# Kernel optimization log

Hardware: AMD Instinct MI355X
Metric: run time of the kernel (lower is better)

Reference implementation:

```python
import jax, jax.numpy as jnp
import numpy as np

B, C, H, W = 4, 192, 128, 128
NH = 6
HD = C // NH            # 32
GS = 8                  # window (group) size
K = 16                  # unfold kernel size
STRIDE, PAD = 8, 4
NUM = H // GS           # 16 groups per side
BG = B * NUM * NUM      # 1024 windows
N = GS * GS             # 64 tokens per group
KK = K * K              # 256 sampled tokens per window
SCALE = HD ** -0.5


def _rope(x):
    # lucidrains-style rotary embedding along dim -2 (positions), last dim = head_dim
    d = x.shape[-1]
    inv = 1.0 / (10000.0 ** (jnp.arange(0, d, 2, dtype=jnp.float32) / d))
    t = jnp.arange(x.shape[-2], dtype=jnp.float32)
    freqs = jnp.repeat(t[:, None] * inv[None, :], 2, axis=-1)  # [seq, d], interleaved
    cos, sin = jnp.cos(freqs), jnp.sin(freqs)
    xp = x.reshape(x.shape[:-1] + (d // 2, 2))
    xr = jnp.stack((-xp[..., 1], xp[..., 0]), axis=-1).reshape(x.shape)
    return x * cos + xr * sin


def _l2norm(x):
    # torch F.normalize(dim=-1): x / max(||x||, eps)
    n = jnp.linalg.norm(x, axis=-1, keepdims=True)
    return x / jnp.maximum(n, 1e-12)


def setup_inputs() -> dict:
    key = jax.random.key(0)
    ks = jax.random.split(key, 6)
    return {
        "x_complete": jax.random.normal(ks[0], (B, C, H, W), jnp.float32),
        "graph": jax.random.randint(ks[1], (BG, 1, N, KK), 0, 2) > 0,
        "w_group": jax.random.normal(ks[2], (C, C), jnp.float32) * 0.02,
        "b_group": jnp.zeros((C,), jnp.float32),
        "w_sample": jax.random.normal(ks[3], (2 * C, C), jnp.float32) * 0.02,
        "b_sample": jnp.zeros((2 * C,), jnp.float32),
        "w_proj": jax.random.normal(ks[4], (C, C), jnp.float32) * 0.02,
        "b_proj": jnp.zeros((C,), jnp.float32),
    }


def reference(x_complete, graph, w_group, b_group, w_sample, b_sample, w_proj, b_proj):
    # --- local grouping: [B,C,(numh sh),(numw sw)] -> [(B numh numw), sh*sw, C]
    xg = x_complete.reshape(B, C, NUM, GS, NUM, GS).transpose(0, 2, 4, 3, 5, 1).reshape(BG, N, C)
    # --- proj_group: 1x1 Conv1d over channels, then split heads 'b (h c) n -> b h n c'
    x1 = jnp.einsum('bnc,dc->bnd', xg, w_group) + b_group
    x1 = x1.reshape(BG, N, NH, HD).transpose(0, 2, 1, 3)            # [BG,NH,N,HD]
    # --- proj_sample: 1x1 Conv2d to 2C channels
    xs = jnp.einsum('bchw,dc->bdhw', x_complete, w_sample) + b_sample[None, :, None, None]
    # --- F.unfold(kernel=16, stride=8, pad=4): patch features channel-major (c,k0,k1)
    patches = jax.lax.conv_general_dilated_patches(
        xs, (K, K), (STRIDE, STRIDE), ((PAD, PAD), (PAD, PAD)))    # [B, 2C*KK, NUM, NUM]
    xs = patches.reshape(B, 2 * C, KK, NUM * NUM).transpose(0, 3, 2, 1).reshape(BG, KK, 2 * C)
    # --- 'b n (div h c) -> div b h n c'
    xs = xs.reshape(BG, KK, 2, NH, HD)
    x2 = xs[:, :, 0].transpose(0, 2, 1, 3)                          # [BG,NH,KK,HD]
    feat = xs[:, :, 1].transpose(0, 2, 1, 3)                        # [BG,NH,KK,HD]
    # --- RoPE + masked cosine-sim attention
    q = _rope(x1)
    k = _rope(x2)
    sim = jnp.einsum('bhmc,bhnc->bhmn', _l2norm(q), _l2norm(k))
    sim = sim + (-100.0) * (~graph).astype(sim.dtype)
    corr = jax.nn.softmax(sim * SCALE, axis=-1)                     # [BG,NH,N,KK]
    out = jnp.einsum('bhmn,bhnc->bhmc', corr, feat)                 # [BG,NH,N,HD]
    out = out.transpose(0, 2, 1, 3).reshape(BG, N, C)
    return out @ w_proj.T + b_proj
```

## Files before the change

### kernel.cpp

```cpp
#include <hip/hip_runtime.h>
#include <hip/hip_bf16.h>

#define B_    4
#define C_    192
#define C2_   384
#define PIX_  16384
#define NH_   6
#define BG_   1024
#define SCALE_ 0.17677669529663687f
#define C1_ 0.2550348943f

typedef __attribute__((ext_vector_type(8))) short short8v;
typedef __attribute__((ext_vector_type(4))) float f32x4;

__global__ __launch_bounds__(256, 1)
void k_rope_init(float2* __restrict__ tbl) {
    int e = blockIdx.x * 256 + threadIdx.x;
    if (e >= 4096) return;
    int pos = e >> 4, j = e & 15;
    float freq = powf(10.0f, -0.25f * (float)j);
    float ang = (float)pos * freq;
    float sn, cs;
    sincosf(ang, &sn, &cs);
    tbl[e] = make_float2(cs, sn);
}

__global__ __launch_bounds__(256, 4)
void k_gmask(const int* __restrict__ g, unsigned int* __restrict__ gbits) {
    int e = blockIdx.x * 256 + threadIdx.x;
    const uint4* p = (const uint4*)(g + (size_t)e * 32);
    unsigned int m = 0u;
#pragma unroll
    for (int i = 0; i < 8; ++i) {
        uint4 v = p[i];
        m |= (v.x ? 1u : 0u) << (i * 4);
        m |= (v.y ? 1u : 0u) << (i * 4 + 1);
        m |= (v.z ? 1u : 0u) << (i * 4 + 2);
        m |= (v.w ? 1u : 0u) << (i * 4 + 3);
    }
    gbits[e] = m;
}

__global__ __launch_bounds__(256, 4)
void k_wcast(const float* __restrict__ wsm, const float* __restrict__ wgb,
             const float* __restrict__ wpj, __hip_bfloat16* __restrict__ wb)
{
    int e = (blockIdx.x * 256 + threadIdx.x) * 4;
    float4 v = (e < 73728) ? *(const float4*)(wsm + e)
             : (e < 110592) ? *(const float4*)(wgb + (e - 73728))
                            : *(const float4*)(wpj + (e - 110592));
    union { uint2 u; __hip_bfloat16 h[4]; } pk;
    pk.h[0] = __float2bfloat16(v.x); pk.h[1] = __float2bfloat16(v.y);
    pk.h[2] = __float2bfloat16(v.z); pk.h[3] = __float2bfloat16(v.w);
    *(uint2*)(wb + e) = pk.u;
}

__global__ __launch_bounds__(256, 4)
void k_convm(const float* __restrict__ x, const __hip_bfloat16* __restrict__ wb,
             const float* __restrict__ bsm, const float* __restrict__ bgb,
             const float2* __restrict__ tbl,
             __hip_bfloat16* __restrict__ xsk, __hip_bfloat16* __restrict__ xsv,
             __hip_bfloat16* __restrict__ qbf)
{
    __shared__ __align__(16) char smem[25600];
    const int bid = blockIdx.x;
    const int b = bid >> 8, pt = bid & 255;
    const int px0 = pt * 64;
    const int t = threadIdx.x;

    {
        const int px = t & 63, cq = t >> 6;
        const float* src = x + ((size_t)b * C_ + cq * 48) * PIX_ + px0 + px;
        char* row = smem + px * 400 + cq * 96;
#pragma unroll
        for (int i = 0; i < 6; ++i) {
            union { uint4 u; __hip_bfloat16 h[8]; } pk;
#pragma unroll
            for (int j = 0; j < 8; ++j)
                pk.h[j] = __float2bfloat16(src[(size_t)(i * 8 + j) * PIX_]);
            *(uint4*)(row + i * 16) = pk.u;
        }
    }
    __syncthreads();

    const int w = t >> 6, lane = t & 63;
    const int l15 = lane & 15, g = lane >> 4;
    const int mb = (w & 1) * 32;
    const int nb = (w >> 1) * 32;

    short8v xf0[6], xf1[6];
#pragma unroll
    for (int ks = 0; ks < 6; ++ks) {
        xf0[ks] = *(const short8v*)(smem + (mb + l15) * 400      + ks * 64 + g * 16);
        xf1[ks] = *(const short8v*)(smem + (mb + 16 + l15) * 400 + ks * 64 + g * 16);
    }

    const f32x4 zz = {0.0f, 0.0f, 0.0f, 0.0f};

#pragma unroll
    for (int o2 = 0; o2 < 3; ++o2) {
        const int oct = 3 + o2;
        f32x4 acc00 = zz, acc01 = zz, acc10 = zz, acc11 = zz;
        const __hip_bfloat16* w0 = wb + (size_t)(oct * 64 + nb + l15) * C_;
        const __hip_bfloat16* w1 = w0 + 16 * C_;
#pragma unroll
        for (int ks = 0; ks < 6; ++ks) {
            const short8v b0 = *(const short8v*)(w0 + ks * 32 + g * 8);
            const short8v b1 = *(const short8v*)(w1 + ks * 32 + g * 8);
            acc00 = __builtin_amdgcn_mfma_f32_16x16x32_bf16(xf0[ks], b0, acc00, 0, 0, 0);
            acc01 = __builtin_amdgcn_mfma_f32_16x16x32_bf16(xf0[ks], b1, acc01, 0, 0, 0);
            acc10 = __builtin_amdgcn_mfma_f32_16x16x32_bf16(xf1[ks], b0, acc10, 0, 0, 0);
            acc11 = __builtin_amdgcn_mfma_f32_16x16x32_bf16(xf1[ks], b1, acc11, 0, 0, 0);
        }
        const float bo0 = bsm[oct * 64 + nb + l15];
        const float bo1 = bsm[oct * 64 + nb + 16 + l15];
        union { uint2 u; __hip_bfloat16 h[4]; } p00, p10, p01, p11;
#pragma unroll
        for (int j = 0; j < 4; ++j) {
            p00.h[j] = __float2bfloat16(acc00[j] + bo0);
            p10.h[j] = __float2bfloat16(acc10[j] + bo0);
            p01.h[j] = __float2bfloat16(acc01[j] + bo1);
            p11.h[j] = __float2bfloat16(acc11[j] + bo1);
        }
        __hip_bfloat16* d0 = xsv + (size_t)(b * C_ + o2 * 64 + nb + l15) * PIX_
                                 + px0 + mb + g * 4;
        *(uint2*)d0        = p00.u;
        *(uint2*)(d0 + 16) = p10.u;
        __hip_bfloat16* d1 = d0 + (size_t)16 * PIX_;
        *(uint2*)d1        = p01.u;
        *(uint2*)(d1 + 16) = p11.u;
    }

#pragma unroll
    for (int o2 = 0; o2 < 3; ++o2) {
        const int oct = o2;
        f32x4 a00 = zz, a01 = zz, a10 = zz, a11 = zz;
        const __hip_bfloat16* w0 = wb + (size_t)(oct * 64 + nb + l15) * C_;
        const __hip_bfloat16* w1 = w0 + 16 * C_;
#pragma unroll
        for (int ks = 0; ks < 6; ++ks) {
            const short8v wf0 = *(const short8v*)(w0 + ks * 32 + g * 8);
            const short8v wf1 = *(const short8v*)(w1 + ks * 32 + g * 8);
            a00 = __builtin_amdgcn_mfma_f32_16x16x32_bf16(wf0, xf0[ks], a00, 0, 0, 0);
            a01 = __builtin_amdgcn_mfma_f32_16x16x32_bf16(wf0, xf1[ks], a01, 0, 0, 0);
            a10 = __builtin_amdgcn_mfma_f32_16x16x32_bf16(wf1, xf0[ks], a10, 0, 0, 0);
            a11 = __builtin_amdgcn_mfma_f32_16x16x32_bf16(wf1, xf1[ks], a11, 0, 0, 0);
        }
        const float4 bv0 = *(const float4*)(bsm + oct * 64 + nb + g * 4);
        const float4 bv1 = *(const float4*)(bsm + oct * 64 + nb + 16 + g * 4);
        a00[0] += bv0.x; a00[1] += bv0.y; a00[2] += bv0.z; a00[3] += bv0.w;
        a01[0] += bv0.x; a01[1] += bv0.y; a01[2] += bv0.z; a01[3] += bv0.w;
        a10[0] += bv1.x; a10[1] += bv1.y; a10[2] += bv1.z; a10[3] += bv1.w;
        a11[0] += bv1.x; a11[1] += bv1.y; a11[2] += bv1.z; a11[3] += bv1.w;
        float s0 = 0.0f, s1 = 0.0f;
#pragma unroll
        for (int j = 0; j < 4; ++j) {
            s0 = fmaf(a00[j], a00[j], s0); s0 = fmaf(a10[j], a10[j], s0);
            s1 = fmaf(a01[j], a01[j], s1); s1 = fmaf(a11[j], a11[j], s1);
        }
        s0 += __shfl_xor(s0, 16); s0 += __shfl_xor(s0, 32);
        s1 += __shfl_xor(s1, 16); s1 += __shfl_xor(s1, 32);
        const float inv0 = 1.0f / fmaxf(sqrtf(s0), 1e-12f);
        const float inv1 = 1.0f / fmaxf(sqrtf(s1), 1e-12f);
        union { uint2 u; __hip_bfloat16 h[4]; } q00, q10, q01, q11;
#pragma unroll
        for (int j = 0; j < 4; ++j) {
            q00.h[j] = __float2bfloat16(a00[j] * inv0);
            q10.h[j] = __float2bfloat16(a10[j] * inv0);
            q01.h[j] = __float2bfloat16(a01[j] * inv1);
            q11.h[j] = __float2bfloat16(a11[j] * inv1);
        }
        __hip_bfloat16* d0 = xsk + ((size_t)b * PIX_ + px0 + mb + l15) * C_
                                 + oct * 64 + nb + g * 4;
        *(uint2*)d0        = q00.u;
        *(uint2*)(d0 + 16) = q10.u;
        __hip_bfloat16* d1 = d0 + (size_t)16 * C_;
        *(uint2*)d1        = q01.u;
        *(uint2*)(d1 + 16) = q11.u;
    }

    const int r = pt >> 1;
    const int c0q = (pt & 1) * 64 + mb + l15;
    const int n0 = (r & 7) * 8 + (c0q & 7);
    const int n1 = (r & 7) * 8 + ((c0q + 16) & 7);
    const int bg0 = (b << 8) + ((r >> 3) << 4) + (c0q >> 3);
    const int bg1 = (b << 8) + ((r >> 3) << 4) + ((c0q + 16) >> 3);
#pragma unroll
    for (int o2 = 0; o2 < 3; ++o2) {
        const int oct = 6 + o2;
        f32x4 a00 = zz, a01 = zz, a10 = zz, a11 = zz;
        const __hip_bfloat16* w0 = wb + (size_t)(oct * 64 + nb + l15) * C_;
        const __hip_bfloat16* w1 = w0 + 16 * C_;
#pragma unroll
        for (int ks = 0; ks < 6; ++ks) {
            const short8v wf0 = *(const short8v*)(w0 + ks * 32 + g * 8);
            const short8v wf1 = *(const short8v*)(w1 + ks * 32 + g * 8);
            a00 = __builtin_amdgcn_mfma_f32_16x16x32_bf16(wf0, xf0[ks], a00, 0, 0, 0);
            a01 = __builtin_amdgcn_mfma_f32_16x16x32_bf16(wf0, xf1[ks], a01, 0, 0, 0);
            a10 = __builtin_amdgcn_mfma_f32_16x16x32_bf16(wf1, xf0[ks], a10, 0, 0, 0);
            a11 = __builtin_amdgcn_mfma_f32_16x16x32_bf16(wf1, xf1[ks], a11, 0, 0, 0);
        }
        const float4 bv0 = *(const float4*)(bgb + (oct - 6) * 64 + nb + g * 4);
        const float4 bv1 = *(const float4*)(bgb + (oct - 6) * 64 + nb + 16 + g * 4);
        a00[0] += bv0.x; a00[1] += bv0.y; a00[2] += bv0.z; a00[3] += bv0.w;
        a01[0] += bv0.x; a01[1] += bv0.y; a01[2] += bv0.z; a01[3] += bv0.w;
        a10[0] += bv1.x; a10[1] += bv1.y; a10[2] += bv1.z; a10[3] += bv1.w;
        a11[0] += bv1.x; a11[1] += bv1.y; a11[2] += bv1.z; a11[3] += bv1.w;
        {
            float2 cA, cB;
            cA = tbl[n0 * 16 + g * 2]; cB = tbl[n0 * 16 + g * 2 + 1];
            { float u0 = a00[0], u1 = a00[1];
              a00[0] = u0 * cA.x - u1 * cA.y; a00[1] = u1 * cA.x + u0 * cA.y; }
            { float u0 = a00[2], u1 = a00[3];
              a00[2] = u0 * cB.x - u1 * cB.y; a00[3] = u1 * cB.x + u0 * cB.y; }
            cA = tbl[n0 * 16 + 8 + g * 2]; cB = tbl[n0 * 16 + 8 + g * 2 + 1];
            { float u0 = a10[0], u1 = a10[1];
              a10[0] = u0 * cA.x - u1 * cA.y; a10[1] = u1 * cA.x + u0 * cA.y; }
            { float u0 = a10[2], u1 = a10[3];
              a10[2] = u0 * cB.x - u1 * cB.y; a10[3] = u1 * cB.x + u0 * cB.y; }
            cA = tbl[n1 * 16 + g * 2]; cB = tbl[n1 * 16 + g * 2 + 1];
            { float u0 = a01[0], u1 = a01[1];
              a01[0] = u0 * cA.x - u1 * cA.y; a01[1] = u1 * cA.x + u0 * cA.y; }
            { float u0 = a01[2], u1 = a01[3];
              a01[2] = u0 * cB.x - u1 * cB.y; a01[3] = u1 * cB.x + u0 * cB.y; }
            cA = tbl[n1 * 16 + 8 + g * 2]; cB = tbl[n1 * 16 + 8 + g * 2 + 1];
            { float u0 = a11[0], u1 = a11[1];
              a11[0] = u0 * cA.x - u1 * cA.y; a11[1] = u1 * cA.x + u0 * cA.y; }
            { float u0 = a11[2], u1 = a11[3];
              a11[2] = u0 * cB.x - u1 * cB.y; a11[3] = u1 * cB.x + u0 * cB.y; }
        }
        float s0 = 0.0f, s1 = 0.0f;
#pragma unroll
        for (int j = 0; j < 4; ++j) {
            s0 = fmaf(a00[j], a00[j], s0); s0 = fmaf(a10[j], a10[j], s0);
            s1 = fmaf(a01[j], a01[j], s1); s1 = fmaf(a11[j], a11[j], s1);
        }
        s0 += __shfl_xor(s0, 16); s0 += __shfl_xor(s0, 32);
        s1 += __shfl_xor(s1, 16); s1 += __shfl_xor(s1, 32);
        const float inv0 = 1.0f / fmaxf(sqrtf(s0), 1e-12f);
        const float inv1 = 1.0f / fmaxf(sqrtf(s1), 1e-12f);
        union { uint2 u; __hip_bfloat16 h[4]; } q00, q10, q01, q11;
#pragma unroll
        for (int j = 0; j < 4; ++j) {
            q00.h[j] = __float2bfloat16(a00[j] * inv0);
            q10.h[j] = __float2bfloat16(a10[j] * inv0);
            q01.h[j] = __float2bfloat16(a01[j] * inv1);
            q11.h[j] = __float2bfloat16(a11[j] * inv1);
        }
        const int hglob = (oct - 6) * 2 + (nb >> 5);
        __hip_bfloat16* d0 = qbf + (((size_t)bg0 * NH_ + hglob) * 64 + n0) * 32 + g * 4;
        *(uint2*)d0        = q00.u;
        *(uint2*)(d0 + 16) = q10.u;
        __hip_bfloat16* d1 = qbf + (((size_t)bg1 * NH_ + hglob) * 64 + n1) * 32 + g * 4;
        *(uint2*)d1        = q01.u;
        *(uint2*)(d1 + 16) = q11.u;
    }
}

__global__ __launch_bounds__(512, 2)
void k_attn(const __hip_bfloat16* __restrict__ xsk, const __hip_bfloat16* __restrict__ xsv,
            const unsigned int* __restrict__ gbits, const __hip_bfloat16* __restrict__ qb,
            const float2* __restrict__ tbl, float* __restrict__ attn)
{
    __shared__ __align__(16) char smem[52736];
    const int bid0 = blockIdx.x;
    const int bid = (bid0 & 7) * 768 + (bid0 >> 3);
    const int h = bid % NH_;
    const int bg = bid / NH_;
    const int b = bg >> 8, ph = (bg >> 4) & 15, pw = bg & 15;
    const int t = threadIdx.x;
    const int w = t >> 6, lane = t & 63;
    const int g = lane >> 4, l15 = lane & 15;
    const int rbase = (w & 3) * 16;
    const int wcol  = w >> 2;
    const int cb    = wcol * 128;
    const int cb32  = wcol * 4;

    const short8v qa = *(const short8v*)(qb +
        ((size_t)(bg * NH_ + h) * 64 + rbase + l15) * 32 + g * 8);

    {
        const int m = t >> 1, half = t & 1;
        const int k0 = m >> 4, k1 = m & 15;
        const int rr = ph * 8 - 4 + k0, cc = pw * 8 - 4 + k1;
        const bool inb = ((unsigned)rr < 128u) && ((unsigned)cc < 128u);
        float kv[16];
        if (inb) {
            const uint4* pk = (const uint4*)(xsk +
                ((size_t)b * PIX_ + rr * 128 + cc) * C_ + h * 32 + half * 16);
            union { uint4 u; __hip_bfloat16 h8[8]; } r0, r1;
            r0.u = pk[0]; r1.u = pk[1];
#pragma unroll
            for (int d = 0; d < 8; ++d) {
                kv[d]     = __bfloat162float(r0.h8[d]);
                kv[8 + d] = __bfloat162float(r1.h8[d]);
            }
        } else {
#pragma unroll
            for (int d = 0; d < 16; ++d) kv[d] = 0.0f;
        }
        union { uint4 u; __hip_bfloat16 hh[8]; } p0, p1;
#pragma unroll
        for (int p = 0; p < 8; ++p) {
            float2 cs = tbl[m * 16 + half * 8 + p];
            float a0 = kv[2 * p], a1 = kv[2 * p + 1];
            float e0 = a0 * cs.x - a1 * cs.y;
            float e1 = a1 * cs.x + a0 * cs.y;
            if (p < 4) { p0.hh[2 * p] = __float2bfloat16(e0); p0.hh[2 * p + 1] = __float2bfloat16(e1); }
            else { p1.hh[2 * (p - 4)] = __float2bfloat16(e0); p1.hh[2 * (p - 4) + 1] = __float2bfloat16(e1); }
        }
        *(uint4*)(smem + m * 80 + half * 32)      = p0.u;
        *(uint4*)(smem + m * 80 + half * 32 + 16) = p1.u;
    }

    {
        const int d = t & 31, k0 = t >> 5;
        const int rr = ph * 8 - 4 + k0;
        const int c0 = pw * 8 - 4;
        char* dst = smem + 34816 + d * 528 + k0 * 32;
        const __hip_bfloat16* src = xsv + (size_t)(b * C_ + h * 32 + d) * PIX_ + rr * 128 + c0;
        const bool rok = (unsigned)rr < 128u;
        if (rok && pw >= 1 && pw <= 14) {
            const uint2* s2 = (const uint2*)src;
            uint2 a0 = s2[0], a1 = s2[1], a2 = s2[2], a3 = s2[3];
            ((uint4*)dst)[0] = make_uint4(a0.x, a0.y, a1.x, a1.y);
            ((uint4*)dst)[1] = make_uint4(a2.x, a2.y, a3.x, a3.y);
        } else {
            __hip_bfloat16* dh = (__hip_bfloat16*)dst;
            __hip_bfloat16 z = __float2bfloat16(0.0f);
#pragma unroll
            for (int i = 0; i < 16; ++i) {
                bool ok = rok && ((unsigned)(c0 + i) < 128u);
                dh[i] = ok ? src[i] : z;
            }
        }
    }

    {
        unsigned int* gbl = (unsigned int*)(smem + 20480);
        const int q = t >> 3, wd = t & 7;
        gbl[q * 9 + wd] = gbits[(size_t)bg * 512 + t];
    }
    __syncthreads();

    f32x4 acc[8];
    const f32x4 zz = {0.0f, 0.0f, 0.0f, 0.0f};
#pragma unroll
    for (int tile = 0; tile < 8; ++tile) {
        const short8v kb = *(const short8v*)(smem + (cb + tile * 16 + l15) * 80 + g * 16);
        acc[tile] = __builtin_amdgcn_mfma_f32_16x16x32_bf16(qa, kb, zz, 0, 0, 0);
    }

    const unsigned int* gbl = (const unsigned int*)(smem + 20480);
    float* reds = (float*)(smem + 51712);
    float sm4[4], inv4[4];
#pragma unroll
    for (int j = 0; j < 4; ++j) {
        const int q = rbase + g * 4 + j;
        const unsigned int wv[4] = { gbl[q * 9 + cb32], gbl[q * 9 + cb32 + 1],
                                     gbl[q * 9 + cb32 + 2], gbl[q * 9 + cb32 + 3] };
        float sm = 0.0f;
#pragma unroll
        for (int tile = 0; tile < 8; ++tile) {
            const unsigned int bit = (wv[tile >> 1] >> ((tile & 1) * 16 + l15)) & 1u;
            float e = __builtin_amdgcn_exp2f(fmaf(acc[tile][j], C1_, -C1_));
            e = bit ? e : 0.0f;
            acc[tile][j] = e;
            sm += e;
        }
        sm += __shfl_xor(sm, 1);
        sm += __shfl_xor(sm, 2);
        sm += __shfl_xor(sm, 4);
        sm += __shfl_xor(sm, 8);
        sm4[j] = sm;
        if (l15 == 0) reds[wcol * 64 + q] = sm;
    }
    __syncthreads();
#pragma unroll
    for (int j = 0; j < 4; ++j) {
        const int q = rbase + g * 4 + j;
        inv4[j] = 1.0f / (sm4[j] + reds[(wcol ^ 1) * 64 + q] + 1e-37f);
    }

    char* plw = smem + w * 4352;
#pragma unroll
    for (int tile = 0; tile < 8; ++tile)
#pragma unroll
        for (int j = 0; j < 4; ++j) {
            *(__hip_bfloat16*)(plw + (g * 4 + j) * 272 + (tile * 16 + l15) * 2) =
                __float2bfloat16(acc[tile][j]);
        }

    f32x4 o0 = zz, o1 = zz;
#pragma unroll
    for (int ks = 0; ks < 4; ++ks) {
        const short8v pa  = *(const short8v*)(plw + l15 * 272 + (ks * 32 + g * 8) * 2);
        const short8v vb0 = *(const short8v*)(smem + 34816 + l15 * 528        + (cb + ks * 32 + g * 8) * 2);
        const short8v vb1 = *(const short8v*)(smem + 34816 + (16 + l15) * 528 + (cb + ks * 32 + g * 8) * 2);
        o0 = __builtin_amdgcn_mfma_f32_16x16x32_bf16(pa, vb0, o0, 0, 0, 0);
        o1 = __builtin_amdgcn_mfma_f32_16x16x32_bf16(pa, vb1, o1, 0, 0, 0);
    }
    __syncthreads();

    float* ob = (float*)smem;
    if (wcol == 1) {
#pragma unroll
        for (int j = 0; j < 4; ++j) {
            const int q = rbase + g * 4 + j;
            ob[q * 33 + l15]      = o0[j];
            ob[q * 33 + 16 + l15] = o1[j];
        }
    }
    __syncthreads();
    if (wcol == 0) {
#pragma unroll
        for (int j = 0; j < 4; ++j) {
            const int q = rbase + g * 4 + j;
            float v0 = (o0[j] + ob[q * 33 + l15])      * inv4[j];
            float v1 = (o1[j] + ob[q * 33 + 16 + l15]) * inv4[j];
            attn[((size_t)bg * 64 + q) * 192 + h * 32 + l15]      = v0;
            attn[((size_t)bg * 64 + q) * 192 + h * 32 + 16 + l15] = v1;
        }
    }
}

__global__ __launch_bounds__(256, 4)
void k_oprojm(const float* __restrict__ attn, const __hip_bfloat16* __restrict__ wpb,
              const float* __restrict__ bp, float* __restrict__ out)
{
    __shared__ __align__(16) char smem[25600];
    const int bid0 = blockIdx.x;
    const int bid = (bid0 & 7) * 384 + (bid0 >> 3);
    const int oct = bid % 3;
    const int rt  = bid / 3;
    const int row0 = rt * 64;
    const int t = threadIdx.x;

#pragma unroll
    for (int e0 = 0; e0 < 12; ++e0) {
        const int e = e0 * 256 + t;
        const int r = e / 48, c4 = e % 48;
        float4 v = *(const float4*)(attn + (size_t)(row0 + r) * 192 + c4 * 4);
        union { uint2 u; __hip_bfloat16 h[4]; } pk;
        pk.h[0] = __float2bfloat16(v.x); pk.h[1] = __float2bfloat16(v.y);
        pk.h[2] = __float2bfloat16(v.z); pk.h[3] = __float2bfloat16(v.w);
        *(uint2*)(smem + r * 400 + c4 * 8) = pk.u;
    }
    __syncthreads();

    const int w = t >> 6, lane = t & 63;
    const int l15 = lane & 15, g = lane >> 4;
    const int mb = (w & 1) * 32;
    const int nb = (w >> 1) * 32;

    const f32x4 zz = {0.0f, 0.0f, 0.0f, 0.0f};
    f32x4 acc00 = zz, acc01 = zz, acc10 = zz, acc11 = zz;
    const __hip_bfloat16* w0 = wpb + (size_t)(oct * 64 + nb + l15) * C_;
    const __hip_bfloat16* w1 = w0 + 16 * C_;
#pragma unroll
    for (int ks = 0; ks < 6; ++ks) {
        const short8v a0 = *(const short8v*)(smem + (mb + l15) * 400      + ks * 64 + g * 16);
        const short8v a1 = *(const short8v*)(smem + (mb + 16 + l15) * 400 + ks * 64 + g * 16);
        const short8v b0 = *(const short8v*)(w0 + ks * 32 + g * 8);
        const short8v b1 = *(const short8v*)(w1 + ks * 32 + g * 8);
        acc00 = __builtin_amdgcn_mfma_f32_16x16x32_bf16(a0, b0, acc00, 0, 0, 0);
        acc01 = __builtin_amdgcn_mfma_f32_16x16x32_bf16(a0, b1, acc01, 0, 0, 0);
        acc10 = __builtin_amdgcn_mfma_f32_16x16x32_bf16(a1, b0, acc10, 0, 0, 0);
        acc11 = __builtin_amdgcn_mfma_f32_16x16x32_bf16(a1, b1, acc11, 0, 0, 0);
    }
    __syncthreads();

    float* ot = (float*)smem;
#pragma unroll
    for (int j = 0; j < 4; ++j) {
        ot[(mb + g * 4 + j) * 68      + nb + l15]      = acc00[j];
        ot[(mb + 16 + g * 4 + j) * 68 + nb + l15]      = acc10[j];
        ot[(mb + g * 4 + j) * 68      + nb + 16 + l15] = acc01[j];
        ot[(mb + 16 + g * 4 + j) * 68 + nb + 16 + l15] = acc11[j];
    }
    __syncthreads();

    {
        const int k = t & 15, pxi = t >> 4;
        const float4 bias4 = *(const float4*)(bp + oct * 64 + k * 4);
#pragma unroll
        for (int p = 0; p < 4; ++p) {
            const int px = p * 16 + pxi;
            float4 v = *(const float4*)&ot[px * 68 + k * 4];
            v.x += bias4.x; v.y += bias4.y; v.z += bias4.z; v.w += bias4.w;
            *(float4*)(out + (size_t)(row0 + px) * 192 + oct * 64 + k * 4) = v;
        }
    }
}

extern "C" void kernel_launch(void* const* d_in, const int* in_sizes, int n_in,
                              void* d_out, int out_size, void* d_ws, size_t ws_size,
                              hipStream_t stream)
{
    (void)in_sizes; (void)n_in; (void)out_size; (void)ws_size;
    const float* x   = (const float*)d_in[0];
    const int* grph  = (const int*)d_in[1];
    const float* wg  = (const float*)d_in[2];
    const float* bgb = (const float*)d_in[3];
    const float* wsm = (const float*)d_in[4];
    const float* bsm = (const float*)d_in[5];
    const float* wp  = (const float*)d_in[6];
    const float* bp  = (const float*)d_in[7];
    float* out = (float*)d_out;

    char* wsb = (char*)d_ws;
    __hip_bfloat16* xsk = (__hip_bfloat16*)wsb;
    __hip_bfloat16* xsv = (__hip_bfloat16*)(wsb + 25165824ull);
    __hip_bfloat16* qbf = (__hip_bfloat16*)(wsb + 50331648ull);
    float2* tbl = (float2*)(wsb + 75497472ull);
    unsigned int* gbits = (unsigned int*)(wsb + 75530240ull);
    __hip_bfloat16* wb  = (__hip_bfloat16*)(wsb + 77627392ull);
    __hip_bfloat16* wpb = wb + 110592;

    hipLaunchKernelGGL(k_rope_init, dim3(16),   dim3(256), 0, stream, tbl);
    hipLaunchKernelGGL(k_wcast,     dim3(144),  dim3(256), 0, stream, wsm, wg, wp, wb);
    hipLaunchKernelGGL(k_gmask,     dim3(2048), dim3(256), 0, stream, grph, gbits);
    hipLaunchKernelGGL(k_convm,     dim3(1024), dim3(256), 0, stream, x, wb, bsm, bgb, tbl, xsk, xsv, qbf);
    hipLaunchKernelGGL(k_attn,      dim3(6144), dim3(512), 0, stream, xsk, xsv, gbits, qbf, tbl, out);
    hipLaunchKernelGGL(k_oprojm,    dim3(3072), dim3(256), 0, stream, out, wpb, bp, out);
}
```

Baseline: 187.4 us.

## Use packed bf16 conversion and transpose score MFMA for row-contiguous softmax

Replaces scalar __float2bfloat16 conversions across all kernels with the v_cvt_pk_bf16_f32 instruction, which converts two floats per instruction. In the attention kernel the score MFMA operands are swapped, so each lane holds four consecutive keys of one query row. This lets the softmax mask use one shifted bitword per tile, cuts the row-sum shuffles from four to two, and stores the probability tile with 8-byte writes instead of scalar bf16 stores. The partial-sum exchange layout in shared memory changes to match, which adds risk around indexing correctness.

```diff
diff --git a/kernel.cpp b/kernel.cpp
--- a/kernel.cpp
+++ b/kernel.cpp
@@ -12,6 +12,12 @@
 
 typedef __attribute__((ext_vector_type(8))) short short8v;
 typedef __attribute__((ext_vector_type(4))) float f32x4;
+
+__device__ __forceinline__ unsigned cvt_pk_bf16(float lo, float hi) {
+    unsigned r;
+    asm("v_cvt_pk_bf16_f32 %0, %1, %2" : "=v"(r) : "v"(lo), "v"(hi));
+    return r;
+}
 
 __global__ __launch_bounds__(256, 1)
 void k_rope_init(float2* __restrict__ tbl) {
@@ -49,10 +55,8 @@
     float4 v = (e < 73728) ? *(const float4*)(wsm + e)
              : (e < 110592) ? *(const float4*)(wgb + (e - 73728))
                             : *(const float4*)(wpj + (e - 110592));
-    union { uint2 u; __hip_bfloat16 h[4]; } pk;
-    pk.h[0] = __float2bfloat16(v.x); pk.h[1] = __float2bfloat16(v.y);
-    pk.h[2] = __float2bfloat16(v.z); pk.h[3] = __float2bfloat16(v.w);
-    *(uint2*)(wb + e) = pk.u;
+    uint2 pk = make_uint2(cvt_pk_bf16(v.x, v.y), cvt_pk_bf16(v.z, v.w));
+    *(uint2*)(wb + e) = pk;
 }
 
 __global__ __launch_bounds__(256, 4)
@@ -74,11 +78,13 @@
         char* row = smem + px * 400 + cq * 96;
 #pragma unroll
         for (int i = 0; i < 6; ++i) {
-            union { uint4 u; __hip_bfloat16 h[8]; } pk;
-#pragma unroll
-            for (int j = 0; j < 8; ++j)
-                pk.h[j] = __float2bfloat16(src[(size_t)(i * 8 + j) * PIX_]);
-            *(uint4*)(row + i * 16) = pk.u;
+            float f[8];
+#pragma unroll
+            for (int j = 0; j < 8; ++j) f[j] = src[(size_t)(i * 8 + j) * PIX_];
+            uint4 pk4;
+            pk4.x = cvt_pk_bf16(f[0], f[1]); pk4.y = cvt_pk_bf16(f[2], f[3]);
+            pk4.z = cvt_pk_bf16(f[4], f[5]); pk4.w = cvt_pk_bf16(f[6], f[7]);
+            *(uint4*)(row + i * 16) = pk4;
         }
     }
     __syncthreads();
@@ -114,21 +120,21 @@
         }
         const float bo0 = bsm[oct * 64 + nb + l15];
         const float bo1 = bsm[oct * 64 + nb + 16 + l15];
-        union { uint2 u; __hip_bfloat16 h[4]; } p00, p10, p01, p11;
-#pragma unroll
-        for (int j = 0; j < 4; ++j) {
-            p00.h[j] = __float2bfloat16(acc00[j] + bo0);
-            p10.h[j] = __float2bfloat16(acc10[j] + bo0);
-            p01.h[j] = __float2bfloat16(acc01[j] + bo1);
-            p11.h[j] = __float2bfloat16(acc11[j] + bo1);
-        }
+        uint2 p00 = make_uint2(cvt_pk_bf16(acc00[0] + bo0, acc00[1] + bo0),
+                               cvt_pk_bf16(acc00[2] + bo0, acc00[3] + bo0));
+        uint2 p10 = make_uint2(cvt_pk_bf16(acc10[0] + bo0, acc10[1] + bo0),
+                               cvt_pk_bf16(acc10[2] + bo0, acc10[3] + bo0));
+        uint2 p01 = make_uint2(cvt_pk_bf16(acc01[0] + bo1, acc01[1] + bo1),
+                               cvt_pk_bf16(acc01[2] + bo1, acc01[3] + bo1));
+        uint2 p11 = make_uint2(cvt_pk_bf16(acc11[0] + bo1, acc11[1] + bo1),
+                               cvt_pk_bf16(acc11[2] + bo1, acc11[3] + bo1));
         __hip_bfloat16* d0 = xsv + (size_t)(b * C_ + o2 * 64 + nb + l15) * PIX_
                                  + px0 + mb + g * 4;
-        *(uint2*)d0        = p00.u;
-        *(uint2*)(d0 + 16) = p10.u;
+        *(uint2*)d0        = p00;
+        *(uint2*)(d0 + 16) = p10;
         __hip_bfloat16* d1 = d0 + (size_t)16 * PIX_;
-        *(uint2*)d1        = p01.u;
-        *(uint2*)(d1 + 16) = p11.u;
+        *(uint2*)d1        = p01;
+        *(uint2*)(d1 + 16) = p11;
     }
 
 #pragma unroll
@@ -162,21 +168,21 @@
         s1 += __shfl_xor(s1, 16); s1 += __shfl_xor(s1, 32);
         const float inv0 = 1.0f / fmaxf(sqrtf(s0), 1e-12f);
         const float inv1 = 1.0f / fmaxf(sqrtf(s1), 1e-12f);
-        union { uint2 u; __hip_bfloat16 h[4]; } q00, q10, q01, q11;
-#pragma unroll
-        for (int j = 0; j < 4; ++j) {
-            q00.h[j] = __float2bfloat16(a00[j] * inv0);
-            q10.h[j] = __float2bfloat16(a10[j] * inv0);
-            q01.h[j] = __float2bfloat16(a01[j] * inv1);
-            q11.h[j] = __float2bfloat16(a11[j] * inv1);
-        }
+        uint2 q00 = make_uint2(cvt_pk_bf16(a00[0] * inv0, a00[1] * inv0),
+                               cvt_pk_bf16(a00[2] * inv0, a00[3] * inv0));
+        uint2 q10 = make_uint2(cvt_pk_bf16(a10[0] * inv0, a10[1] * inv0),
+                               cvt_pk_bf16(a10[2] * inv0, a10[3] * inv0));
+        uint2 q01 = make_uint2(cvt_pk_bf16(a01[0] * inv1, a01[1] * inv1),
+                               cvt_pk_bf16(a01[2] * inv1, a01[3] * inv1));
+        uint2 q11 = make_uint2(cvt_pk_bf16(a11[0] * inv1, a11[1] * inv1),
+                               cvt_pk_bf16(a11[2] * inv1, a11[3] * inv1));
         __hip_bfloat16* d0 = xsk + ((size_t)b * PIX_ + px0 + mb + l15) * C_
                                  + oct * 64 + nb + g * 4;
-        *(uint2*)d0        = q00.u;
-        *(uint2*)(d0 + 16) = q10.u;
+        *(uint2*)d0        = q00;
+        *(uint2*)(d0 + 16) = q10;
         __hip_bfloat16* d1 = d0 + (size_t)16 * C_;
-        *(uint2*)d1        = q01.u;
-        *(uint2*)(d1 + 16) = q11.u;
+        *(uint2*)d1        = q01;
+        *(uint2*)(d1 + 16) = q11;
     }
 
     const int r = pt >> 1;
@@ -239,21 +245,21 @@
         s1 += __shfl_xor(s1, 16); s1 += __shfl_xor(s1, 32);
         const float inv0 = 1.0f / fmaxf(sqrtf(s0), 1e-12f);
         const float inv1 = 1.0f / fmaxf(sqrtf(s1), 1e-12f);
-        union { uint2 u; __hip_bfloat16 h[4]; } q00, q10, q01, q11;
-#pragma unroll
-        for (int j = 0; j < 4; ++j) {
-            q00.h[j] = __float2bfloat16(a00[j] * inv0);
-            q10.h[j] = __float2bfloat16(a10[j] * inv0);
-            q01.h[j] = __float2bfloat16(a01[j] * inv1);
-            q11.h[j] = __float2bfloat16(a11[j] * inv1);
-        }
+        uint2 q00 = make_uint2(cvt_pk_bf16(a00[0] * inv0, a00[1] * inv0),
+                               cvt_pk_bf16(a00[2] * inv0, a00[3] * inv0));
+        uint2 q10 = make_uint2(cvt_pk_bf16(a10[0] * inv0, a10[1] * inv0),
+                               cvt_pk_bf16(a10[2] * inv0, a10[3] * inv0));
+        uint2 q01 = make_uint2(cvt_pk_bf16(a01[0] * inv1, a01[1] * inv1),
+                               cvt_pk_bf16(a01[2] * inv1, a01[3] * inv1));
+        uint2 q11 = make_uint2(cvt_pk_bf16(a11[0] * inv1, a11[1] * inv1),
+                               cvt_pk_bf16(a11[2] * inv1, a11[3] * inv1));
         const int hglob = (oct - 6) * 2 + (nb >> 5);
         __hip_bfloat16* d0 = qbf + (((size_t)bg0 * NH_ + hglob) * 64 + n0) * 32 + g * 4;
-        *(uint2*)d0        = q00.u;
-        *(uint2*)(d0 + 16) = q10.u;
+        *(uint2*)d0        = q00;
+        *(uint2*)(d0 + 16) = q10;
         __hip_bfloat16* d1 = qbf + (((size_t)bg1 * NH_ + hglob) * 64 + n1) * 32 + g * 4;
-        *(uint2*)d1        = q01.u;
-        *(uint2*)(d1 + 16) = q11.u;
+        *(uint2*)d1        = q01;
+        *(uint2*)(d1 + 16) = q11;
     }
 }
 
@@ -299,18 +305,17 @@
 #pragma unroll
             for (int d = 0; d < 16; ++d) kv[d] = 0.0f;
         }
-        union { uint4 u; __hip_bfloat16 hh[8]; } p0, p1;
+        unsigned pk8[8];
 #pragma unroll
         for (int p = 0; p < 8; ++p) {
             float2 cs = tbl[m * 16 + half * 8 + p];
             float a0 = kv[2 * p], a1 = kv[2 * p + 1];
             float e0 = a0 * cs.x - a1 * cs.y;
             float e1 = a1 * cs.x + a0 * cs.y;
-            if (p < 4) { p0.hh[2 * p] = __float2bfloat16(e0); p0.hh[2 * p + 1] = __float2bfloat16(e1); }
-            else { p1.hh[2 * (p - 4)] = __float2bfloat16(e0); p1.hh[2 * (p - 4) + 1] = __float2bfloat16(e1); }
-        }
-        *(uint4*)(smem + m * 80 + half * 32)      = p0.u;
-        *(uint4*)(smem + m * 80 + half * 32 + 16) = p1.u;
+            pk8[p] = cvt_pk_bf16(e0, e1);
+        }
+        *(uint4*)(smem + m * 80 + half * 32)      = make_uint4(pk8[0], pk8[1], pk8[2], pk8[3]);
+        *(uint4*)(smem + m * 80 + half * 32 + 16) = make_uint4(pk8[4], pk8[5], pk8[6], pk8[7]);
     }
 
     {
@@ -348,48 +353,48 @@
 #pragma unroll
     for (int tile = 0; tile < 8; ++tile) {
         const short8v kb = *(const short8v*)(smem + (cb + tile * 16 + l15) * 80 + g * 16);
-        acc[tile] = __builtin_amdgcn_mfma_f32_16x16x32_bf16(qa, kb, zz, 0, 0, 0);
+        acc[tile] = __builtin_amdgcn_mfma_f32_16x16x32_bf16(kb, qa, zz, 0, 0, 0);
     }
 
     const unsigned int* gbl = (const unsigned int*)(smem + 20480);
     float* reds = (float*)(smem + 51712);
-    float sm4[4], inv4[4];
-#pragma unroll
-    for (int j = 0; j < 4; ++j) {
-        const int q = rbase + g * 4 + j;
+    {
+        const int q = rbase + l15;
         const unsigned int wv[4] = { gbl[q * 9 + cb32], gbl[q * 9 + cb32 + 1],
                                      gbl[q * 9 + cb32 + 2], gbl[q * 9 + cb32 + 3] };
         float sm = 0.0f;
 #pragma unroll
         for (int tile = 0; tile < 8; ++tile) {
-            const unsigned int bit = (wv[tile >> 1] >> ((tile & 1) * 16 + l15)) & 1u;
-            float e = __builtin_amdgcn_exp2f(fmaf(acc[tile][j], C1_, -C1_));
-            e = bit ? e : 0.0f;
-            acc[tile][j] = e;
-            sm += e;
-        }
-        sm += __shfl_xor(sm, 1);
-        sm += __shfl_xor(sm, 2);
-        sm += __shfl_xor(sm, 4);
-        sm += __shfl_xor(sm, 8);
-        sm4[j] = sm;
-        if (l15 == 0) reds[wcol * 64 + q] = sm;
-    }
-    __syncthreads();
+            const unsigned int bits = wv[tile >> 1] >> ((tile & 1) * 16 + (g << 2));
+#pragma unroll
+            for (int j = 0; j < 4; ++j) {
+                float e = __builtin_amdgcn_exp2f(fmaf(acc[tile][j], C1_, -C1_));
+                e = ((bits >> j) & 1u) ? e : 0.0f;
+                acc[tile][j] = e;
+                sm += e;
+            }
+        }
+        sm += __shfl_xor(sm, 16);
+        sm += __shfl_xor(sm, 32);
+        if (lane < 16) reds[q * 2 + wcol] = sm;
+    }
+    __syncthreads();
+
+    float inv4[4];
 #pragma unroll
     for (int j = 0; j < 4; ++j) {
-        const int q = rbase + g * 4 + j;
-        inv4[j] = 1.0f / (sm4[j] + reds[(wcol ^ 1) * 64 + q] + 1e-37f);
+        const int qq = rbase + (g << 2) + j;
+        float2 rr2 = *(const float2*)&reds[qq * 2];
+        inv4[j] = 1.0f / (rr2.x + rr2.y + 1e-37f);
     }
 
     char* plw = smem + w * 4352;
 #pragma unroll
-    for (int tile = 0; tile < 8; ++tile)
-#pragma unroll
-        for (int j = 0; j < 4; ++j) {
-            *(__hip_bfloat16*)(plw + (g * 4 + j) * 272 + (tile * 16 + l15) * 2) =
-                __float2bfloat16(acc[tile][j]);
-        }
+    for (int tile = 0; tile < 8; ++tile) {
+        uint2 pw2 = make_uint2(cvt_pk_bf16(acc[tile][0], acc[tile][1]),
+                               cvt_pk_bf16(acc[tile][2], acc[tile][3]));
+        *(uint2*)(plw + l15 * 272 + tile * 32 + g * 8) = pw2;
+    }
 
     f32x4 o0 = zz, o1 = zz;
 #pragma unroll
@@ -441,10 +446,8 @@
         const int e = e0 * 256 + t;
         const int r = e / 48, c4 = e % 48;
         float4 v = *(const float4*)(attn + (size_t)(row0 + r) * 192 + c4 * 4);
-        union { uint2 u; __hip_bfloat16 h[4]; } pk;
-        pk.h[0] = __float2bfloat16(v.x); pk.h[1] = __float2bfloat16(v.y);
-        pk.h[2] = __float2bfloat16(v.z); pk.h[3] = __float2bfloat16(v.w);
-        *(uint2*)(smem + r * 400 + c4 * 8) = pk.u;
+        uint2 pk = make_uint2(cvt_pk_bf16(v.x, v.y), cvt_pk_bf16(v.z, v.w));
+        *(uint2*)(smem + r * 400 + c4 * 8) = pk;
     }
     __syncthreads();
 
```

Result: no change. 186.0 us (-0.8%).
